# Performance work log

Measured on AMD Instinct MI355X. Metric: run time of the kernel, lower is better.

The kernel has to match this reference:

```python
import jax, jax.numpy as jnp
import numpy as np

SCALE = 0.08838834764831845  # 1/sqrt(128)


def setup_inputs() -> dict:
    key = jax.random.key(0)
    k1, k2, k3, k4 = jax.random.split(key, 4)
    B, Sq, H, D = 1, 2048, 32, 128
    Skv, K = 4096, 256
    return {
        "q": jax.random.normal(k1, (B, Sq, H, D), jnp.float32),
        "kv": jax.random.normal(k2, (B, Skv, 2, D), jnp.float32),  # stacked K,V (MQA)
        "attn_sink": jax.random.normal(k3, (H,), jnp.float32),
        "topk_idxs": jax.random.randint(k4, (B, Sq, K), 0, Skv),
    }


def reference(q, kv, attn_sink, topk_idxs):
    # q:        [B, Sq, H, D]
    # kv:       [B, Skv, 2, D]  (index 0 = keys, 1 = values; shared across heads)
    # topk_idxs:[B, Sq, K]      per-query selected KV positions
    # attn_sink:[H]             per-head sink logit added to the softmax denominator
    B = q.shape[0]
    # Gather selected KV per query: [B, Sq, K, 2, D]
    gathered = kv[jnp.arange(B)[:, None, None], topk_idxs]
    k = gathered[..., 0, :]  # [B, Sq, K, D]
    v = gathered[..., 1, :]  # [B, Sq, K, D]

    scores = jnp.einsum("bqhd,bqkd->bqhk", q, k) * SCALE  # [B, Sq, H, K]
    sink = attn_sink[None, None, :, None]                  # [1, 1, H, 1]

    # Numerically stable softmax over K selected tokens + sink logit.
    m = jnp.maximum(jnp.max(scores, axis=-1, keepdims=True), sink)
    e = jnp.exp(scores - m)
    denom = jnp.sum(e, axis=-1, keepdims=True) + jnp.exp(sink - m)
    probs = e / denom                                      # sink absorbs leftover mass

    out = jnp.einsum("bqhk,bqkd->bqhd", probs, v)          # [B, Sq, H, D]
    return out
```

## Files before the change

### kernel.cpp

```cpp
#include <hip/hip_runtime.h>
#include <hip/hip_bf16.h>

#define SQ 2048
#define NH 32
#define DH 128
#define NK 256
#define SCALE 0.08838834764831845f
#define LOG2E 1.4426950408889634f

typedef __attribute__((ext_vector_type(8))) __bf16 bf16x8;
typedef __attribute__((ext_vector_type(4))) float floatx4;

#define VB_STRIDE 72
#define PB_STRIDE 264

#define OFF_VB   16896
#define OFF_RED  35328
#define OFF_RED2 35840
#define SMEM_SZ  36352

__device__ __forceinline__ unsigned pk_bf16(float a, float b) {
  union { __hip_bfloat162 h2; unsigned u; } c;
  c.h2 = __float22bfloat162_rn(make_float2(a, b));
  return c.u;
}

__device__ __forceinline__ float fast_exp2(float x) {
#if __has_builtin(__builtin_amdgcn_exp2f)
  return __builtin_amdgcn_exp2f(x);
#else
  return exp2f(x);
#endif
}

template <int CTRL>
__device__ __forceinline__ float dpp_rot(float x) {
  int i = __builtin_bit_cast(int, x);
  i = __builtin_amdgcn_mov_dpp(i, CTRL, 0xF, 0xF, true);
  return __builtin_bit_cast(float, i);
}
#define RED16_MAX(v) { v = fmaxf(v, dpp_rot<0x121>(v)); v = fmaxf(v, dpp_rot<0x122>(v)); \
                       v = fmaxf(v, dpp_rot<0x124>(v)); v = fmaxf(v, dpp_rot<0x128>(v)); }
#define RED16_SUM(v) { v += dpp_rot<0x121>(v); v += dpp_rot<0x122>(v); \
                       v += dpp_rot<0x124>(v); v += dpp_rot<0x128>(v); }

__global__ __launch_bounds__(256) void kv_to_bf16(const float* __restrict__ kv,
                                                  unsigned short* __restrict__ kvb) {
  int i = blockIdx.x * 256 + threadIdx.x;
  float4 f = ((const float4*)kv)[i];
  uint2 o = { pk_bf16(f.x, f.y), pk_bf16(f.z, f.w) };
  ((uint2*)kvb)[i] = o;
}

struct VR { uint4 a, b, c, d; };

__device__ __forceinline__ VR v_load(const unsigned short* __restrict__ kvb,
                                     const int* __restrict__ tkg, int c, int tid) {
  int rg = tid & 15, dg = tid >> 4;
  int r0 = rg * 4, d0 = dg * 8;
  int4 i4 = *(const int4*)&tkg[c * 64 + r0];
  VR v;
  v.a = *(const uint4*)(kvb + (size_t)i4.x * 256 + 128 + d0);
  v.b = *(const uint4*)(kvb + (size_t)i4.y * 256 + 128 + d0);
  v.c = *(const uint4*)(kvb + (size_t)i4.z * 256 + 128 + d0);
  v.d = *(const uint4*)(kvb + (size_t)i4.w * 256 + 128 + d0);
  return v;
}

__device__ __forceinline__ void v_write(unsigned short* vbuf, const VR& v, int tid) {
  int rg = tid & 15, dg = tid >> 4;
  int r0 = rg * 4, d0 = dg * 8;
  const unsigned* pa = (const unsigned*)&v.a;
  const unsigned* pb = (const unsigned*)&v.b;
  const unsigned* pc = (const unsigned*)&v.c;
  const unsigned* pd = (const unsigned*)&v.d;
#pragma unroll
  for (int w = 0; w < 4; w++) {
    unsigned lo01 = __builtin_amdgcn_perm(pb[w], pa[w], 0x05040100u);
    unsigned lo23 = __builtin_amdgcn_perm(pd[w], pc[w], 0x05040100u);
    unsigned hi01 = __builtin_amdgcn_perm(pb[w], pa[w], 0x07060302u);
    unsigned hi23 = __builtin_amdgcn_perm(pd[w], pc[w], 0x07060302u);
    uint2 lo = { lo01, lo23 }, hi = { hi01, hi23 };
    *(uint2*)&vbuf[(d0 + 2 * w) * VB_STRIDE + r0] = lo;
    *(uint2*)&vbuf[(d0 + 2 * w + 1) * VB_STRIDE + r0] = hi;
  }
}

__device__ __forceinline__ void gemm1_direct(const unsigned short* __restrict__ kvb,
                                             int idx, const bf16x8 af[2][4], int quad,
                                             floatx4& a0, floatx4& a1) {
  const unsigned short* kp = kvb + (size_t)idx * 256 + quad * 8;
  a0 = (floatx4){0.f, 0.f, 0.f, 0.f};
  a1 = (floatx4){0.f, 0.f, 0.f, 0.f};
#pragma unroll
  for (int ks = 0; ks < 4; ks++) {
    bf16x8 b = *(const bf16x8*)(kp + ks * 32);
    a0 = __builtin_amdgcn_mfma_f32_16x16x32_bf16(af[0][ks], b, a0, 0, 0, 0);
    a1 = __builtin_amdgcn_mfma_f32_16x16x32_bf16(af[1][ks], b, a1, 0, 0, 0);
  }
}

__device__ __forceinline__ void pv_chunk(const unsigned short* pbuf,
                                         const unsigned short* vbuf, int c,
                                         int wave, int quad, int l16,
                                         floatx4 oacc[2][2]) {
#pragma unroll
  for (int ks = 0; ks < 2; ks++) {
    int kof = c * 64 + ks * 32 + quad * 8;
    bf16x8 a0 = *(const bf16x8*)&pbuf[l16 * PB_STRIDE + kof];
    bf16x8 a1 = *(const bf16x8*)&pbuf[(16 + l16) * PB_STRIDE + kof];
    int kl = ks * 32 + quad * 8;
    bf16x8 b0 = *(const bf16x8*)&vbuf[(wave * 32 + l16) * VB_STRIDE + kl];
    bf16x8 b1 = *(const bf16x8*)&vbuf[(wave * 32 + 16 + l16) * VB_STRIDE + kl];
    oacc[0][0] = __builtin_amdgcn_mfma_f32_16x16x32_bf16(a0, b0, oacc[0][0], 0, 0, 0);
    oacc[0][1] = __builtin_amdgcn_mfma_f32_16x16x32_bf16(a0, b1, oacc[0][1], 0, 0, 0);
    oacc[1][0] = __builtin_amdgcn_mfma_f32_16x16x32_bf16(a1, b0, oacc[1][0], 0, 0, 0);
    oacc[1][1] = __builtin_amdgcn_mfma_f32_16x16x32_bf16(a1, b1, oacc[1][1], 0, 0, 0);
  }
}

__global__ __launch_bounds__(256, 4) void sparse_attn_kernel(
    const float* __restrict__ q, const unsigned short* __restrict__ kvb,
    const float* __restrict__ sink, const int* __restrict__ topk,
    float* __restrict__ out) {
  __shared__ __align__(16) char smem[SMEM_SZ];
  unsigned short* pbuf = (unsigned short*)smem;
  unsigned short* vbuf = (unsigned short*)(smem + OFF_VB);
  float* red  = (float*)(smem + OFF_RED);
  float* red2 = (float*)(smem + OFF_RED2);

  const int tid = threadIdx.x;
  const int s = blockIdx.x;
  const int wave = tid >> 6;
  const int lane = tid & 63;
  const int quad = lane >> 4;
  const int l16 = lane & 15;
  const int* tkg = topk + (size_t)s * NK;

  float snk[2][4];
#pragma unroll
  for (int mt = 0; mt < 2; mt++)
#pragma unroll
    for (int r = 0; r < 4; r++)
      snk[mt][r] = sink[mt * 16 + quad * 4 + r] * LOG2E;

  int kidx[4];
#pragma unroll
  for (int c = 0; c < 4; c++) kidx[c] = tkg[c * 64 + wave * 16 + l16];

  const float QSC = SCALE * LOG2E;
  const float* qp = q + (size_t)s * (NH * DH);
  bf16x8 afrag[2][4];
#pragma unroll
  for (int mt = 0; mt < 2; mt++)
#pragma unroll
    for (int ks = 0; ks < 4; ks++) {
      const float* base = qp + (mt * 16 + l16) * DH + ks * 32 + quad * 8;
      float4 f0 = ((const float4*)base)[0];
      float4 f1 = ((const float4*)base)[1];
      uint4 u = { pk_bf16(f0.x * QSC, f0.y * QSC), pk_bf16(f0.z * QSC, f0.w * QSC),
                  pk_bf16(f1.x * QSC, f1.y * QSC), pk_bf16(f1.z * QSC, f1.w * QSC) };
      afrag[mt][ks] = __builtin_bit_cast(bf16x8, u);
    }

  floatx4 sc[4][2];
  gemm1_direct(kvb, kidx[0], afrag, quad, sc[0][0], sc[0][1]);
  VR v0 = v_load(kvb, tkg, 0, tid);
  gemm1_direct(kvb, kidx[1], afrag, quad, sc[1][0], sc[1][1]);
  v_write(vbuf, v0, tid);
  gemm1_direct(kvb, kidx[2], afrag, quad, sc[2][0], sc[2][1]);
  VR v1 = v_load(kvb, tkg, 1, tid);
  gemm1_direct(kvb, kidx[3], afrag, quad, sc[3][0], sc[3][1]);

  float mh[2][4];
#pragma unroll
  for (int mt = 0; mt < 2; mt++)
#pragma unroll
    for (int r = 0; r < 4; r++) {
      float v = fmaxf(fmaxf(sc[0][mt][r], sc[1][mt][r]),
                      fmaxf(sc[2][mt][r], sc[3][mt][r]));
      RED16_MAX(v);
      mh[mt][r] = v;
    }
  if (l16 == 0) {
#pragma unroll
    for (int mt = 0; mt < 2; mt++)
#pragma unroll
      for (int r = 0; r < 4; r++)
        red[wave * 32 + mt * 16 + quad * 4 + r] = mh[mt][r];
  }
  __syncthreads();
#pragma unroll
  for (int mt = 0; mt < 2; mt++)
#pragma unroll
    for (int r = 0; r < 4; r++) {
      int h = mt * 16 + quad * 4 + r;
      float v = snk[mt][r];
#pragma unroll
      for (int w = 0; w < 4; w++) v = fmaxf(v, red[w * 32 + h]);
      mh[mt][r] = v;
    }
  float ps[2][4];
#pragma unroll
  for (int mt = 0; mt < 2; mt++)
#pragma unroll
    for (int r = 0; r < 4; r++) {
      float acc = 0.f;
#pragma unroll
      for (int c = 0; c < 4; c++) {
        float e = fast_exp2(sc[c][mt][r] - mh[mt][r]);
        sc[c][mt][r] = e;
        acc += e;
      }
      RED16_SUM(acc);
      ps[mt][r] = acc;
    }
  if (l16 == 0) {
#pragma unroll
    for (int mt = 0; mt < 2; mt++)
#pragma unroll
      for (int r = 0; r < 4; r++)
        red2[wave * 32 + mt * 16 + quad * 4 + r] = ps[mt][r];
  }
  __syncthreads();
  float inv[2][4];
#pragma unroll
  for (int mt = 0; mt < 2; mt++)
#pragma unroll
    for (int r = 0; r < 4; r++) {
      float dd = fast_exp2(snk[mt][r] - mh[mt][r]);
#pragma unroll
      for (int w = 0; w < 4; w++) dd += red2[w * 32 + mt * 16 + quad * 4 + r];
      inv[mt][r] = 1.0f / dd;
    }
#pragma unroll
  for (int c = 0; c < 4; c++)
#pragma unroll
    for (int mt = 0; mt < 2; mt++) {
      int col = c * 64 + wave * 16 + l16;
      unsigned short* pb = &pbuf[(mt * 16 + quad * 4) * PB_STRIDE + col];
      unsigned p01 = pk_bf16(sc[c][mt][0], sc[c][mt][1]);
      unsigned p23 = pk_bf16(sc[c][mt][2], sc[c][mt][3]);
      pb[0] = (unsigned short)p01;
      pb[PB_STRIDE] = (unsigned short)(p01 >> 16);
      pb[2 * PB_STRIDE] = (unsigned short)p23;
      pb[3 * PB_STRIDE] = (unsigned short)(p23 >> 16);
    }
  __syncthreads();

  floatx4 oacc[2][2];
#pragma unroll
  for (int mt = 0; mt < 2; mt++)
#pragma unroll
    for (int nt = 0; nt < 2; nt++)
      oacc[mt][nt] = (floatx4){0.f, 0.f, 0.f, 0.f};

  pv_chunk(pbuf, vbuf, 0, wave, quad, l16, oacc);
  __syncthreads();
  v_write(vbuf, v1, tid);
  VR v2 = v_load(kvb, tkg, 2, tid);
  __syncthreads();

  pv_chunk(pbuf, vbuf, 1, wave, quad, l16, oacc);
  __syncthreads();
  v_write(vbuf, v2, tid);
  VR v3 = v_load(kvb, tkg, 3, tid);
  __syncthreads();

  pv_chunk(pbuf, vbuf, 2, wave, quad, l16, oacc);
  __syncthreads();
  v_write(vbuf, v3, tid);
  __syncthreads();

  pv_chunk(pbuf, vbuf, 3, wave, quad, l16, oacc);

  {
    float* op = out + (size_t)s * (NH * DH);
#pragma unroll
    for (int mt = 0; mt < 2; mt++)
#pragma unroll
      for (int nt = 0; nt < 2; nt++)
#pragma unroll
        for (int r4 = 0; r4 < 4; r4++) {
          int h = mt * 16 + quad * 4 + r4;
          int d = wave * 32 + nt * 16 + l16;
          op[h * DH + d] = oacc[mt][nt][r4] * inv[mt][r4];
        }
  }
}

extern "C" void kernel_launch(void* const* d_in, const int* in_sizes, int n_in,
                              void* d_out, int out_size, void* d_ws, size_t ws_size,
                              hipStream_t stream) {
  (void)in_sizes; (void)n_in; (void)out_size; (void)ws_size;
  const float* q    = (const float*)d_in[0];
  const float* kv   = (const float*)d_in[1];
  const float* sink = (const float*)d_in[2];
  const int*   topk = (const int*)d_in[3];
  float* out = (float*)d_out;
  unsigned short* kvb = (unsigned short*)d_ws;

  kv_to_bf16<<<dim3(1024), dim3(256), 0, stream>>>(kv, kvb);
  sparse_attn_kernel<<<dim3(SQ), dim3(256), 0, stream>>>(q, kvb, sink, topk, out);
}
```

Baseline: 129.4 us.

## Prefetch K fragments and V chunks earlier, raise wave priority around MFMAs

Splits the K-gather from the QK^T MFMAs so K rows for chunks 0 and 1 are loaded up front, together with the Q loads, and later chunks are double-buffered in registers one step ahead. V chunk loads 2 and 3 are issued earlier, during the softmax and before the first PV chunk. s_setprio is raised around the MFMA sections. The aim is to hide gather latency, at the cost of more live registers, which could cause spills or lower occupancy under launch_bounds(256,4).

```diff
diff --git a/kernel.cpp b/kernel.cpp
--- a/kernel.cpp
+++ b/kernel.cpp
@@ -86,24 +86,35 @@
   }
 }
 
-__device__ __forceinline__ void gemm1_direct(const unsigned short* __restrict__ kvb,
-                                             int idx, const bf16x8 af[2][4], int quad,
-                                             floatx4& a0, floatx4& a1) {
+struct KB { bf16x8 b[4]; };
+
+__device__ __forceinline__ KB kb_load(const unsigned short* __restrict__ kvb,
+                                      int idx, int quad) {
   const unsigned short* kp = kvb + (size_t)idx * 256 + quad * 8;
+  KB k;
+#pragma unroll
+  for (int ks = 0; ks < 4; ks++) k.b[ks] = *(const bf16x8*)(kp + ks * 32);
+  return k;
+}
+
+__device__ __forceinline__ void gemm_reg(const KB& kb, const bf16x8 af[2][4],
+                                         floatx4& a0, floatx4& a1) {
   a0 = (floatx4){0.f, 0.f, 0.f, 0.f};
   a1 = (floatx4){0.f, 0.f, 0.f, 0.f};
+  __builtin_amdgcn_s_setprio(1);
 #pragma unroll
   for (int ks = 0; ks < 4; ks++) {
-    bf16x8 b = *(const bf16x8*)(kp + ks * 32);
-    a0 = __builtin_amdgcn_mfma_f32_16x16x32_bf16(af[0][ks], b, a0, 0, 0, 0);
-    a1 = __builtin_amdgcn_mfma_f32_16x16x32_bf16(af[1][ks], b, a1, 0, 0, 0);
-  }
+    a0 = __builtin_amdgcn_mfma_f32_16x16x32_bf16(af[0][ks], kb.b[ks], a0, 0, 0, 0);
+    a1 = __builtin_amdgcn_mfma_f32_16x16x32_bf16(af[1][ks], kb.b[ks], a1, 0, 0, 0);
+  }
+  __builtin_amdgcn_s_setprio(0);
 }
 
 __device__ __forceinline__ void pv_chunk(const unsigned short* pbuf,
                                          const unsigned short* vbuf, int c,
                                          int wave, int quad, int l16,
                                          floatx4 oacc[2][2]) {
+  __builtin_amdgcn_s_setprio(1);
 #pragma unroll
   for (int ks = 0; ks < 2; ks++) {
     int kof = c * 64 + ks * 32 + quad * 8;
@@ -117,6 +128,7 @@
     oacc[1][0] = __builtin_amdgcn_mfma_f32_16x16x32_bf16(a1, b0, oacc[1][0], 0, 0, 0);
     oacc[1][1] = __builtin_amdgcn_mfma_f32_16x16x32_bf16(a1, b1, oacc[1][1], 0, 0, 0);
   }
+  __builtin_amdgcn_s_setprio(0);
 }
 
 __global__ __launch_bounds__(256, 4) void sparse_attn_kernel(
@@ -137,6 +149,26 @@
   const int l16 = lane & 15;
   const int* tkg = topk + (size_t)s * NK;
 
+  const float QSC = SCALE * LOG2E;
+  const float* qp = q + (size_t)s * (NH * DH);
+  float4 qf[2][4][2];
+#pragma unroll
+  for (int mt = 0; mt < 2; mt++)
+#pragma unroll
+    for (int ks = 0; ks < 4; ks++) {
+      const float* base = qp + (mt * 16 + l16) * DH + ks * 32 + quad * 8;
+      qf[mt][ks][0] = ((const float4*)base)[0];
+      qf[mt][ks][1] = ((const float4*)base)[1];
+    }
+
+  int kidx[4];
+#pragma unroll
+  for (int c = 0; c < 4; c++) kidx[c] = tkg[c * 64 + wave * 16 + l16];
+
+  KB b0 = kb_load(kvb, kidx[0], quad);
+  KB b1 = kb_load(kvb, kidx[1], quad);
+  VR v0 = v_load(kvb, tkg, 0, tid);
+
   float snk[2][4];
 #pragma unroll
   for (int mt = 0; mt < 2; mt++)
@@ -144,33 +176,26 @@
     for (int r = 0; r < 4; r++)
       snk[mt][r] = sink[mt * 16 + quad * 4 + r] * LOG2E;
 
-  int kidx[4];
-#pragma unroll
-  for (int c = 0; c < 4; c++) kidx[c] = tkg[c * 64 + wave * 16 + l16];
-
-  const float QSC = SCALE * LOG2E;
-  const float* qp = q + (size_t)s * (NH * DH);
   bf16x8 afrag[2][4];
 #pragma unroll
   for (int mt = 0; mt < 2; mt++)
 #pragma unroll
     for (int ks = 0; ks < 4; ks++) {
-      const float* base = qp + (mt * 16 + l16) * DH + ks * 32 + quad * 8;
-      float4 f0 = ((const float4*)base)[0];
-      float4 f1 = ((const float4*)base)[1];
+      float4 f0 = qf[mt][ks][0], f1 = qf[mt][ks][1];
       uint4 u = { pk_bf16(f0.x * QSC, f0.y * QSC), pk_bf16(f0.z * QSC, f0.w * QSC),
                   pk_bf16(f1.x * QSC, f1.y * QSC), pk_bf16(f1.z * QSC, f1.w * QSC) };
       afrag[mt][ks] = __builtin_bit_cast(bf16x8, u);
     }
 
   floatx4 sc[4][2];
-  gemm1_direct(kvb, kidx[0], afrag, quad, sc[0][0], sc[0][1]);
-  VR v0 = v_load(kvb, tkg, 0, tid);
-  gemm1_direct(kvb, kidx[1], afrag, quad, sc[1][0], sc[1][1]);
+  gemm_reg(b0, afrag, sc[0][0], sc[0][1]);
+  KB b2 = kb_load(kvb, kidx[2], quad);
   v_write(vbuf, v0, tid);
-  gemm1_direct(kvb, kidx[2], afrag, quad, sc[2][0], sc[2][1]);
+  gemm_reg(b1, afrag, sc[1][0], sc[1][1]);
+  KB b3 = kb_load(kvb, kidx[3], quad);
+  gemm_reg(b2, afrag, sc[2][0], sc[2][1]);
   VR v1 = v_load(kvb, tkg, 1, tid);
-  gemm1_direct(kvb, kidx[3], afrag, quad, sc[3][0], sc[3][1]);
+  gemm_reg(b3, afrag, sc[3][0], sc[3][1]);
 
   float mh[2][4];
 #pragma unroll
@@ -190,6 +215,7 @@
         red[wave * 32 + mt * 16 + quad * 4 + r] = mh[mt][r];
   }
   __syncthreads();
+  VR v2 = v_load(kvb, tkg, 2, tid);
 #pragma unroll
   for (int mt = 0; mt < 2; mt++)
 #pragma unroll
@@ -255,16 +281,15 @@
     for (int nt = 0; nt < 2; nt++)
       oacc[mt][nt] = (floatx4){0.f, 0.f, 0.f, 0.f};
 
+  VR v3 = v_load(kvb, tkg, 3, tid);
   pv_chunk(pbuf, vbuf, 0, wave, quad, l16, oacc);
   __syncthreads();
   v_write(vbuf, v1, tid);
-  VR v2 = v_load(kvb, tkg, 2, tid);
   __syncthreads();
 
   pv_chunk(pbuf, vbuf, 1, wave, quad, l16, oacc);
   __syncthreads();
   v_write(vbuf, v2, tid);
-  VR v3 = v_load(kvb, tkg, 3, tid);
   __syncthreads();
 
   pv_chunk(pbuf, vbuf, 2, wave, quad, l16, oacc);
```

New measurement: 130.1 us. No clear change (+0.5%).

## Stage K through double-buffered LDS and merge softmax reductions into one barrier

Applied to the files above, without the earlier changes.

Gathered K rows are now loaded cooperatively, each thread reading a 64-byte contiguous row segment, and staged into double-buffered LDS. The next chunk is prefetched while MFMAs run on the current one. Before, each wave read its K operands straight from global memory. Q is converted once through an LDS tile, V chunks use the same double buffers, the per-wave max and sum are combined with a single barrier using rescaling, and MFMA sections get raised wave priority. The larger LDS footprint lowers the occupancy target from 4 to 3 blocks per CU, and the V buffer overlaps the reduction scratch, which relies on the barrier ordering to stay safe.

```diff
diff --git a/kernel.cpp b/kernel.cpp
--- a/kernel.cpp
+++ b/kernel.cpp
@@ -11,13 +11,19 @@
 typedef __attribute__((ext_vector_type(8))) __bf16 bf16x8;
 typedef __attribute__((ext_vector_type(4))) float floatx4;
 
+#define QS_STRIDE 136
+#define KS_STRIDE 136
 #define VB_STRIDE 72
 #define PB_STRIDE 264
 
-#define OFF_VB   16896
-#define OFF_RED  35328
-#define OFF_RED2 35840
-#define SMEM_SZ  36352
+#define OFF_DB0  16896
+#define DBSZ     18432
+#define OFF_DB1  (OFF_DB0 + DBSZ)
+#define OFF_RED  (OFF_DB1 + 17408)
+#define OFF_RED2 (OFF_RED + 512)
+#define SMEM_SZ  53760
+
+#define SCHED_PIN() __builtin_amdgcn_sched_barrier(0)
 
 __device__ __forceinline__ unsigned pk_bf16(float a, float b) {
   union { __hip_bfloat162 h2; unsigned u; } c;
@@ -52,7 +58,26 @@
   ((uint2*)kvb)[i] = o;
 }
 
+struct KR { uint4 v[4]; };
 struct VR { uint4 a, b, c, d; };
+
+__device__ __forceinline__ KR k_load(const unsigned short* __restrict__ kvb,
+                                     const int* __restrict__ tkg, int c, int tid) {
+  int r = tid >> 2, seg = tid & 3;
+  int idx = tkg[c * 64 + r];
+  const uint4* p = (const uint4*)(kvb + (size_t)idx * 256 + seg * 32);
+  KR k;
+#pragma unroll
+  for (int i = 0; i < 4; i++) k.v[i] = p[i];
+  return k;
+}
+
+__device__ __forceinline__ void k_write(unsigned short* kbuf, const KR& k, int tid) {
+  int r = tid >> 2, seg = tid & 3;
+  uint4* d = (uint4*)&kbuf[r * KS_STRIDE + seg * 32];
+#pragma unroll
+  for (int i = 0; i < 4; i++) d[i] = k.v[i];
+}
 
 __device__ __forceinline__ VR v_load(const unsigned short* __restrict__ kvb,
                                      const int* __restrict__ tkg, int c, int tid) {
@@ -86,24 +111,26 @@
   }
 }
 
-__device__ __forceinline__ void gemm1_direct(const unsigned short* __restrict__ kvb,
-                                             int idx, const bf16x8 af[2][4], int quad,
-                                             floatx4& a0, floatx4& a1) {
-  const unsigned short* kp = kvb + (size_t)idx * 256 + quad * 8;
+__device__ __forceinline__ void gemm1(const unsigned short* kbuf,
+                                      const bf16x8 af[2][4], int nrow, int quad,
+                                      floatx4& a0, floatx4& a1) {
   a0 = (floatx4){0.f, 0.f, 0.f, 0.f};
   a1 = (floatx4){0.f, 0.f, 0.f, 0.f};
+  __builtin_amdgcn_s_setprio(1);
 #pragma unroll
   for (int ks = 0; ks < 4; ks++) {
-    bf16x8 b = *(const bf16x8*)(kp + ks * 32);
+    bf16x8 b = *(const bf16x8*)&kbuf[nrow * KS_STRIDE + ks * 32 + quad * 8];
     a0 = __builtin_amdgcn_mfma_f32_16x16x32_bf16(af[0][ks], b, a0, 0, 0, 0);
     a1 = __builtin_amdgcn_mfma_f32_16x16x32_bf16(af[1][ks], b, a1, 0, 0, 0);
   }
+  __builtin_amdgcn_s_setprio(0);
 }
 
 __device__ __forceinline__ void pv_chunk(const unsigned short* pbuf,
                                          const unsigned short* vbuf, int c,
                                          int wave, int quad, int l16,
                                          floatx4 oacc[2][2]) {
+  __builtin_amdgcn_s_setprio(1);
 #pragma unroll
   for (int ks = 0; ks < 2; ks++) {
     int kof = c * 64 + ks * 32 + quad * 8;
@@ -117,15 +144,18 @@
     oacc[1][0] = __builtin_amdgcn_mfma_f32_16x16x32_bf16(a1, b0, oacc[1][0], 0, 0, 0);
     oacc[1][1] = __builtin_amdgcn_mfma_f32_16x16x32_bf16(a1, b1, oacc[1][1], 0, 0, 0);
   }
-}
-
-__global__ __launch_bounds__(256, 4) void sparse_attn_kernel(
+  __builtin_amdgcn_s_setprio(0);
+}
+
+__global__ __launch_bounds__(256, 3) void sparse_attn_kernel(
     const float* __restrict__ q, const unsigned short* __restrict__ kvb,
     const float* __restrict__ sink, const int* __restrict__ topk,
     float* __restrict__ out) {
   __shared__ __align__(16) char smem[SMEM_SZ];
   unsigned short* pbuf = (unsigned short*)smem;
-  unsigned short* vbuf = (unsigned short*)(smem + OFF_VB);
+  unsigned short* qs   = (unsigned short*)smem;
+  unsigned short* db0  = (unsigned short*)(smem + OFF_DB0);
+  unsigned short* db1  = (unsigned short*)(smem + OFF_DB1);
   float* red  = (float*)(smem + OFF_RED);
   float* red2 = (float*)(smem + OFF_RED2);
 
@@ -136,6 +166,18 @@
   const int quad = lane >> 4;
   const int l16 = lane & 15;
   const int* tkg = topk + (size_t)s * NK;
+  unsigned short* dbuf[2] = { db0, db1 };
+
+  {
+    int r = tid >> 2, seg = tid & 3;
+    int idx = tkg[r];
+    const uint4* p = (const uint4*)(kvb + (size_t)idx * 256 + seg * 32);
+    uint4* d = (uint4*)&db0[r * KS_STRIDE + seg * 32];
+#pragma unroll
+    for (int i = 0; i < 4; i++) d[i] = p[i];
+  }
+  KR k1 = k_load(kvb, tkg, 1, tid);
+  SCHED_PIN();
 
   float snk[2][4];
 #pragma unroll
@@ -144,33 +186,54 @@
     for (int r = 0; r < 4; r++)
       snk[mt][r] = sink[mt * 16 + quad * 4 + r] * LOG2E;
 
-  int kidx[4];
-#pragma unroll
-  for (int c = 0; c < 4; c++) kidx[c] = tkg[c * 64 + wave * 16 + l16];
-
-  const float QSC = SCALE * LOG2E;
-  const float* qp = q + (size_t)s * (NH * DH);
+  {
+    const float QSC = SCALE * LOG2E;
+    const float* qp = q + (size_t)s * (NH * DH);
+    int h = tid >> 3, d0 = (tid & 7) * 16;
+    const float4* src = (const float4*)(qp + h * DH + d0);
+    float4 f0 = src[0], f1 = src[1], f2 = src[2], f3 = src[3];
+    uint4 o0 = { pk_bf16(f0.x * QSC, f0.y * QSC), pk_bf16(f0.z * QSC, f0.w * QSC),
+                 pk_bf16(f1.x * QSC, f1.y * QSC), pk_bf16(f1.z * QSC, f1.w * QSC) };
+    uint4 o1 = { pk_bf16(f2.x * QSC, f2.y * QSC), pk_bf16(f2.z * QSC, f2.w * QSC),
+                 pk_bf16(f3.x * QSC, f3.y * QSC), pk_bf16(f3.z * QSC, f3.w * QSC) };
+    *(uint4*)&qs[h * QS_STRIDE + d0] = o0;
+    *(uint4*)&qs[h * QS_STRIDE + d0 + 8] = o1;
+  }
+  __syncthreads();
+
   bf16x8 afrag[2][4];
 #pragma unroll
   for (int mt = 0; mt < 2; mt++)
 #pragma unroll
-    for (int ks = 0; ks < 4; ks++) {
-      const float* base = qp + (mt * 16 + l16) * DH + ks * 32 + quad * 8;
-      float4 f0 = ((const float4*)base)[0];
-      float4 f1 = ((const float4*)base)[1];
-      uint4 u = { pk_bf16(f0.x * QSC, f0.y * QSC), pk_bf16(f0.z * QSC, f0.w * QSC),
-                  pk_bf16(f1.x * QSC, f1.y * QSC), pk_bf16(f1.z * QSC, f1.w * QSC) };
-      afrag[mt][ks] = __builtin_bit_cast(bf16x8, u);
-    }
+    for (int ks = 0; ks < 4; ks++)
+      afrag[mt][ks] =
+          *(const bf16x8*)&qs[(mt * 16 + l16) * QS_STRIDE + ks * 32 + quad * 8];
+
+  const int nrow = wave * 16 + l16;
 
   floatx4 sc[4][2];
-  gemm1_direct(kvb, kidx[0], afrag, quad, sc[0][0], sc[0][1]);
+  KR k2 = k_load(kvb, tkg, 2, tid);
+  SCHED_PIN();
+  gemm1(dbuf[0], afrag, nrow, quad, sc[0][0], sc[0][1]);
+  k_write(dbuf[1], k1, tid);
+  __syncthreads();
+
+  KR k3 = k_load(kvb, tkg, 3, tid);
+  SCHED_PIN();
+  gemm1(dbuf[1], afrag, nrow, quad, sc[1][0], sc[1][1]);
+  k_write(dbuf[0], k2, tid);
+  __syncthreads();
+
   VR v0 = v_load(kvb, tkg, 0, tid);
-  gemm1_direct(kvb, kidx[1], afrag, quad, sc[1][0], sc[1][1]);
-  v_write(vbuf, v0, tid);
-  gemm1_direct(kvb, kidx[2], afrag, quad, sc[2][0], sc[2][1]);
+  SCHED_PIN();
+  gemm1(dbuf[0], afrag, nrow, quad, sc[2][0], sc[2][1]);
+  k_write(dbuf[1], k3, tid);
+  __syncthreads();
+
   VR v1 = v_load(kvb, tkg, 1, tid);
-  gemm1_direct(kvb, kidx[3], afrag, quad, sc[3][0], sc[3][1]);
+  SCHED_PIN();
+  gemm1(dbuf[1], afrag, nrow, quad, sc[3][0], sc[3][1]);
+  v_write(dbuf[0], v0, tid);
 
   float mh[2][4];
 #pragma unroll
@@ -180,24 +243,6 @@
       float v = fmaxf(fmaxf(sc[0][mt][r], sc[1][mt][r]),
                       fmaxf(sc[2][mt][r], sc[3][mt][r]));
       RED16_MAX(v);
-      mh[mt][r] = v;
-    }
-  if (l16 == 0) {
-#pragma unroll
-    for (int mt = 0; mt < 2; mt++)
-#pragma unroll
-      for (int r = 0; r < 4; r++)
-        red[wave * 32 + mt * 16 + quad * 4 + r] = mh[mt][r];
-  }
-  __syncthreads();
-#pragma unroll
-  for (int mt = 0; mt < 2; mt++)
-#pragma unroll
-    for (int r = 0; r < 4; r++) {
-      int h = mt * 16 + quad * 4 + r;
-      float v = snk[mt][r];
-#pragma unroll
-      for (int w = 0; w < 4; w++) v = fmaxf(v, red[w * 32 + h]);
       mh[mt][r] = v;
     }
   float ps[2][4];
@@ -219,19 +264,29 @@
 #pragma unroll
     for (int mt = 0; mt < 2; mt++)
 #pragma unroll
-      for (int r = 0; r < 4; r++)
+      for (int r = 0; r < 4; r++) {
+        red[wave * 32 + mt * 16 + quad * 4 + r]  = mh[mt][r];
         red2[wave * 32 + mt * 16 + quad * 4 + r] = ps[mt][r];
-  }
-  __syncthreads();
-  float inv[2][4];
+      }
+  }
+  __syncthreads();
+  VR v2 = v_load(kvb, tkg, 2, tid);
+  SCHED_PIN();
+  float inv[2][4], sf[2][4];
 #pragma unroll
   for (int mt = 0; mt < 2; mt++)
 #pragma unroll
     for (int r = 0; r < 4; r++) {
-      float dd = fast_exp2(snk[mt][r] - mh[mt][r]);
-#pragma unroll
-      for (int w = 0; w < 4; w++) dd += red2[w * 32 + mt * 16 + quad * 4 + r];
+      int h = mt * 16 + quad * 4 + r;
+      float M = snk[mt][r];
+#pragma unroll
+      for (int w = 0; w < 4; w++) M = fmaxf(M, red[w * 32 + h]);
+      float dd = fast_exp2(snk[mt][r] - M);
+#pragma unroll
+      for (int w = 0; w < 4; w++)
+        dd += red2[w * 32 + h] * fast_exp2(red[w * 32 + h] - M);
       inv[mt][r] = 1.0f / dd;
+      sf[mt][r] = fast_exp2(mh[mt][r] - M);
     }
 #pragma unroll
   for (int c = 0; c < 4; c++)
@@ -239,8 +294,8 @@
     for (int mt = 0; mt < 2; mt++) {
       int col = c * 64 + wave * 16 + l16;
       unsigned short* pb = &pbuf[(mt * 16 + quad * 4) * PB_STRIDE + col];
-      unsigned p01 = pk_bf16(sc[c][mt][0], sc[c][mt][1]);
-      unsigned p23 = pk_bf16(sc[c][mt][2], sc[c][mt][3]);
+      unsigned p01 = pk_bf16(sc[c][mt][0] * sf[mt][0], sc[c][mt][1] * sf[mt][1]);
+      unsigned p23 = pk_bf16(sc[c][mt][2] * sf[mt][2], sc[c][mt][3] * sf[mt][3]);
       pb[0] = (unsigned short)p01;
       pb[PB_STRIDE] = (unsigned short)(p01 >> 16);
       pb[2 * PB_STRIDE] = (unsigned short)p23;
@@ -255,24 +310,21 @@
     for (int nt = 0; nt < 2; nt++)
       oacc[mt][nt] = (floatx4){0.f, 0.f, 0.f, 0.f};
 
-  pv_chunk(pbuf, vbuf, 0, wave, quad, l16, oacc);
-  __syncthreads();
-  v_write(vbuf, v1, tid);
-  VR v2 = v_load(kvb, tkg, 2, tid);
-  __syncthreads();
-
-  pv_chunk(pbuf, vbuf, 1, wave, quad, l16, oacc);
-  __syncthreads();
-  v_write(vbuf, v2, tid);
   VR v3 = v_load(kvb, tkg, 3, tid);
-  __syncthreads();
-
-  pv_chunk(pbuf, vbuf, 2, wave, quad, l16, oacc);
-  __syncthreads();
-  v_write(vbuf, v3, tid);
-  __syncthreads();
-
-  pv_chunk(pbuf, vbuf, 3, wave, quad, l16, oacc);
+  SCHED_PIN();
+  pv_chunk(pbuf, dbuf[0], 0, wave, quad, l16, oacc);
+  v_write(dbuf[1], v1, tid);
+  __syncthreads();
+
+  pv_chunk(pbuf, dbuf[1], 1, wave, quad, l16, oacc);
+  v_write(dbuf[0], v2, tid);
+  __syncthreads();
+
+  pv_chunk(pbuf, dbuf[0], 2, wave, quad, l16, oacc);
+  v_write(dbuf[1], v3, tid);
+  __syncthreads();
+
+  pv_chunk(pbuf, dbuf[1], 3, wave, quad, l16, oacc);
 
   {
     float* op = out + (size_t)s * (NH * DH);
```

New measurement: 117.6 us. 9.1% less time.
